# Kernel tuning notes

Measured on AMD Instinct MI355X. Metric: run time of the kernel, lower is better.

## Reference

```python
import jax, jax.numpy as jnp
import numpy as np

LMAX = 6; MMAX = 2
C = 128          # num_channels
H = 8            # num_heads
ALPHA = 32       # attn_alpha_channels
VAL = 16         # attn_value_channels (H*VAL == C)
HID = 64         # attn_hidden_channels
FFN = 128        # ffn_hidden_channels
NL = 4           # num_layers
CUTOFF = 12.0; NRBF = 600
AVG_DEG = 23.395238876342773
AVG_NODES = 77.81317
EPS = 1e-16

def _maps():
    idx, ls = [], []
    for l in range(LMAX + 1):
        mm = min(l, MMAX)
        for m in range(-mm, mm + 1):
            idx.append(l * l + l + m); ls.append(l)
    return np.array(idx), np.array(ls)
_M2F_np, _LOF_np = _maps()
M2F = jnp.asarray(_M2F_np)   # [KM] full-coefficient index of each m-restricted coeff
LOF = jnp.asarray(_LOF_np)   # [KM] degree l of each m-restricted coeff
KM = int(_M2F_np.shape[0])   # 29 for lmax=6, mmax=2
KF = (LMAX + 1) ** 2         # 49

def _rbf(d):
    # GaussianSmearing(0, cutoff, NRBF, width_scalar=2.0)
    off = jnp.linspace(0.0, CUTOFF, NRBF)
    coeff = -0.5 / (2.0 * (off[1] - off[0])) ** 2
    return jnp.exp(coeff * (d[:, None] - off) ** 2)

def _envelope(d):
    # PolynomialEnvelope, exponent p=5
    x = d / CUTOFF
    env = 1.0 - 21.0 * x ** 5 + 35.0 * x ** 6 - 15.0 * x ** 7
    return jnp.where(x < 1.0, env, 0.0)

def _rms(x, g):
    # merge-norm over channel dim with learned per-channel scale
    return x * jax.lax.rsqrt(jnp.mean(x * x, axis=-1, keepdims=True) + 1e-6) * g

def _forward(atomic_numbers, edge_index, edge_distance, emb,
             We0, be0, We1, be1, Weproj, gamma1, gamma2,
             Wr0, Wr1, Wrl, Wmsg, Wap, wa, Wg, Wv, Wo,
             Wf1, Wfg, Wf2, Wh1, Wh2):
    N = atomic_numbers.shape[0]
    src, tgt = edge_index[0], edge_index[1]
    rbf = _rbf(edge_distance)            # [E, NRBF]
    env = _envelope(edge_distance)       # [E]
    # node init: atom embedding on the l=0 component
    x = jnp.zeros((N, KF, C), rbf.dtype).at[:, 0, :].set(emb[atomic_numbers])
    # edge-degree embedding: radial MLP -> per-edge coeffs -> scatter to targets
    h = jax.nn.silu(rbf @ We0 + be0)
    h = jax.nn.silu(h @ We1 + be1)
    deg = (h @ Weproj).reshape(-1, KM, C)              # [E, KM, C]
    x = x.at[tgt[:, None], M2F[None, :], :].add(deg / AVG_DEG)
    for i in range(NL):
        # ---- equivariant graph attention ----
        y = _rms(x, gamma1[i])
        ym = y[:, M2F, :]                               # [N, KM, C] m-restricted
        m = jnp.concatenate([ym[src], ym[tgt]], axis=-1)  # [E, KM, 2C]
        m = jnp.einsum('ekc,ch->ekh', m, Wmsg[i])       # [E, KM, HID]
        # radial function, shared across m within each l (use_rad_l_parametrization)
        rad = jax.nn.silu(jax.nn.silu(rbf @ Wr0[i]) @ Wr1[i])
        radl = rad @ Wrl[i]                             # [E, LMAX+1]
        m = m * radl[:, LOF][..., None]
        # attention logits from invariant (l=0) part
        a = jax.nn.silu(m[:, 0, :] @ Wap[i]).reshape(-1, H, ALPHA)
        logits = jnp.einsum('eha,ha->eh', a, wa[i])     # [E, H]
        segmax = jnp.full((N, H), -jnp.inf, logits.dtype).at[tgt].max(logits)
        ex = env[:, None] * jnp.exp(logits - segmax[tgt])  # envelope-masked softmax
        den = jax.ops.segment_sum(ex, tgt, num_segments=N)
        attn = ex / (den[tgt] + EPS)                    # [E, H]
        # SwiGLU-gated equivariant values
        g = jax.nn.silu(m[:, 0, :] @ Wg[i])             # [E, H*VAL]
        v = jnp.einsum('ekh,hv->ekv', m, Wv[i]) * g[:, None, :]
        v = v.reshape(-1, KM, H, VAL) * attn[:, None, :, None]
        agg = jax.ops.segment_sum(v.reshape(-1, KM, H * VAL), tgt, num_segments=N)
        out = jnp.einsum('nkv,vc->nkc', agg, Wo[i])     # [N, KM, C]
        x = x.at[:, M2F, :].add(out)
        # ---- feed-forward (grid-MLP style SwiGLU) ----
        y = _rms(x, gamma2[i])
        gf = jax.nn.silu(y[:, 0, :] @ Wfg[i])           # [N, FFN]
        hf = jnp.einsum('nkc,cf->nkf', y, Wf1[i]) * gf[:, None, :]
        x = x + jnp.einsum('nkf,fc->nkc', hf, Wf2[i])
    # energy head on invariant part, sum-aggregated over nodes
    s = jax.nn.silu(x[:, 0, :] @ Wh1) @ Wh2             # [N, 1]
    return (jnp.sum(s) / AVG_NODES).reshape(1)

def setup_inputs() -> dict:
    key = jax.random.key(0)
    ks = jax.random.split(key, 24)
    N, E = 6000, 120000
    def rn(k, shape, scale=0.05):
        return jax.random.normal(k, shape, dtype=jnp.float32) * scale
    inp = {}
    inp['atomic_numbers'] = jax.random.randint(ks[0], (N,), 0, 128)
    inp['edge_index'] = jax.random.randint(ks[1], (2, E), 0, N)
    inp['edge_distance'] = jax.random.uniform(ks[2], (E,), minval=0.5, maxval=CUTOFF, dtype=jnp.float32)
    inp['emb'] = rn(ks[3], (128, C), 1.0)
    inp['We0'] = rn(ks[4], (NRBF, 128)); inp['be0'] = jnp.zeros((128,), jnp.float32)
    inp['We1'] = rn(ks[5], (128, 128)); inp['be1'] = jnp.zeros((128,), jnp.float32)
    inp['Weproj'] = rn(ks[6], (128, KM * C))
    inp['gamma1'] = jnp.ones((NL, C), jnp.float32)
    inp['gamma2'] = jnp.ones((NL, C), jnp.float32)
    inp['Wr0'] = rn(ks[7], (NL, NRBF, 128))
    inp['Wr1'] = rn(ks[8], (NL, 128, 128))
    inp['Wrl'] = rn(ks[9], (NL, 128, LMAX + 1), 0.1)
    inp['Wmsg'] = rn(ks[10], (NL, 2 * C, HID))
    inp['Wap'] = rn(ks[11], (NL, HID, H * ALPHA))
    inp['wa'] = rn(ks[12], (NL, H, ALPHA))
    inp['Wg'] = rn(ks[13], (NL, HID, H * VAL))
    inp['Wv'] = rn(ks[14], (NL, HID, H * VAL))
    inp['Wo'] = rn(ks[15], (NL, H * VAL, C))
    inp['Wf1'] = rn(ks[16], (NL, C, FFN))
    inp['Wfg'] = rn(ks[17], (NL, C, FFN))
    inp['Wf2'] = rn(ks[18], (NL, FFN, C))
    inp['Wh1'] = rn(ks[19], (C, C))
    inp['Wh2'] = rn(ks[20], (C, 1))
    return inp

def reference(atomic_numbers, edge_index, edge_distance, emb,
              We0, be0, We1, be1, Weproj, gamma1, gamma2,
              Wr0, Wr1, Wrl, Wmsg, Wap, wa, Wg, Wv, Wo,
              Wf1, Wfg, Wf2, Wh1, Wh2):
    return _forward(atomic_numbers, edge_index, edge_distance, emb,
                    We0, be0, We1, be1, Weproj, gamma1, gamma2,
                    Wr0, Wr1, Wrl, Wmsg, Wap, wa, Wg, Wv, Wo,
                    Wf1, Wfg, Wf2, Wh1, Wh2)
```

## Files before the change

kernel.cpp:

```cpp
#include <hip/hip_runtime.h>

#define KM 29
#define GTAB 4096

typedef __bf16 bf16_t;
typedef __bf16 bf16x8 __attribute__((ext_vector_type(8)));
typedef __bf16 bf16x4 __attribute__((ext_vector_type(4)));
typedef float  f32x4  __attribute__((ext_vector_type(4)));
typedef float  f32x2  __attribute__((ext_vector_type(2)));

__device__ __forceinline__ float silu_f(float x){ return x / (1.0f + __expf(-x)); }

__device__ __forceinline__ float wave_reduce_sum(float v){
  #pragma unroll
  for (int s = 1; s < 64; s <<= 1) v += __shfl_xor(v, s);
  return v;
}

__device__ __forceinline__ constexpr int LOF2(int k){
  return (k<1)?0 : (k<4)?1 : (k<9)?2 : (k<14)?3 : (k<19)?4 : (k<24)?5 : 6;
}

__device__ __forceinline__ f32x4 mfma16(bf16x8 a, bf16x8 b, f32x4 c){
  return __builtin_amdgcn_mfma_f32_16x16x32_bf16(a, b, c, 0, 0, 0);
}

__device__ __forceinline__ float env_f(float d){
  float xx = d*(1.0f/12.0f);
  float x2 = xx*xx, x4 = x2*x2, x5 = x4*xx;
  float env = 1.0f - 21.0f*x5 + 35.0f*x5*xx - 15.0f*x5*x2;
  return (xx < 1.0f) ? env : 0.0f;
}

__global__ void k_count(const int* __restrict__ EI, int* __restrict__ cnt, int E){
  int e = blockIdx.x*256 + threadIdx.x;
  if (e < E) atomicAdd(&cnt[EI[E+e]], 1);
}

__global__ __launch_bounds__(1024) void k_scan(int* __restrict__ cnt, int* __restrict__ rowptr, int N){
  __shared__ int ts[1024];
  int t = threadIdx.x;
  int base = t*8;
  int loc[8]; int sum = 0;
  #pragma unroll
  for (int u = 0; u < 8; u++){ int idx = base+u; int v = (idx < N) ? cnt[idx] : 0; loc[u] = sum; sum += v; }
  ts[t] = sum; __syncthreads();
  for (int off = 1; off < 1024; off <<= 1){
    int v = (t >= off) ? ts[t-off] : 0;
    __syncthreads();
    ts[t] += v;
    __syncthreads();
  }
  int excl = ts[t] - sum;
  #pragma unroll
  for (int u = 0; u < 8; u++){
    int idx = base+u;
    if (idx < N){ int r = excl + loc[u]; rowptr[idx] = r; cnt[idx] = r; }
  }
  if (t == 1023) rowptr[N] = ts[1023];
}

__global__ void k_fill(const int* __restrict__ EI, int* __restrict__ cur, int* __restrict__ order, int E){
  int e = blockIdx.x*256 + threadIdx.x;
  if (e < E){ int pos = atomicAdd(&cur[EI[E+e]], 1); order[pos] = e; }
}

__global__ void k_sort(const int* __restrict__ rowptr, int* __restrict__ order, int N){
  int n = blockIdx.x*256 + threadIdx.x;
  if (n >= N) return;
  int rp = rowptr[n], re = rowptr[n+1];
  for (int a = rp+1; a < re; a++){
    int key = order[a]; int b = a-1;
    while (b >= rp && order[b] > key){ order[b+1] = order[b]; b--; }
    order[b+1] = key;
  }
}

__global__ void k_tr(const float* __restrict__ src, bf16_t* __restrict__ dst,
                     int L, int R, int C, int Lstr){
  int idx = blockIdx.x*256 + threadIdx.x;
  int total = L*R*C;
  if (idx >= total) return;
  int l = idx / (R*C); int rem = idx - l*(R*C);
  int r = rem / C; int c = rem - r*C;
  dst[((size_t)l*C + c)*R + r] = (bf16_t)src[(size_t)l*Lstr + (size_t)r*C + c];
}

__global__ void k_tr2(const float* __restrict__ src, bf16_t* __restrict__ dst){
  int idx = blockIdx.x*256 + threadIdx.x;
  if (idx >= 4*128*128) return;
  int l = idx >> 14; int j = (idx >> 7) & 127; int c = idx & 127;
  float v = (j < 64) ? src[(size_t)l*16384 + c*64 + j]
                     : src[(size_t)l*16384 + 8192 + c*64 + (j-64)];
  dst[idx] = (bf16_t)v;
}

__global__ __launch_bounds__(256) void k_tab_embed(
    const float* __restrict__ We0, const float* __restrict__ be0,
    const float* __restrict__ We1, const float* __restrict__ be1,
    const float* __restrict__ Wr0, const float* __restrict__ Wr1, const float* __restrict__ Wrl,
    float* __restrict__ h2tab, float* __restrict__ radtab)
{
  __shared__ float sb[4][640];
  const int wid = threadIdx.x >> 6, lane = threadIdx.x & 63;
  const int e = blockIdx.x*4 + wid;
  if (e >= GTAB) return;
  const float d = e * (12.0f/(GTAB-1));
  const float DLT = 12.0f/599.0f;
  const float CO  = -0.5f/((2.0f*DLT)*(2.0f*DLT));
  int jc = (int)(d/DLT + 0.5f);
  int j0 = jc - 16; if (j0 < 0) j0 = 0; if (j0 > 600-32) j0 = 600-32;
  float diff = d - (float)(j0+lane)*DLT;
  float gval = __expf(CO*diff*diff);
  float p[10];
  #pragma unroll
  for (int u = 0; u < 10; u++) p[u] = 0.f;
  const int c2 = 2*lane;
  for (int jj = 0; jj < 32; jj++){
    float gj = __shfl(gval, jj);
    int row = j0 + jj;
    const float2 w0 = *(const float2*)(We0 + row*128 + c2);
    p[0] += gj*w0.x; p[1] += gj*w0.y;
    #pragma unroll
    for (int i = 0; i < 4; i++){
      const float2 wr = *(const float2*)(Wr0 + ((size_t)i*600 + row)*128 + c2);
      p[2+2*i] += gj*wr.x; p[3+2*i] += gj*wr.y;
    }
  }
  sb[wid][c2]   = silu_f(p[0] + be0[c2]);
  sb[wid][c2+1] = silu_f(p[1] + be0[c2+1]);
  #pragma unroll
  for (int i = 0; i < 4; i++){
    sb[wid][128 + 128*i + c2]   = silu_f(p[2+2*i]);
    sb[wid][128 + 128*i + c2+1] = silu_f(p[3+2*i]);
  }
  float a0 = 0.f, a1 = 0.f;
  for (int c = 0; c < 128; c++){
    float hv = sb[wid][c];
    const float2 w = *(const float2*)(We1 + c*128 + c2);
    a0 += hv*w.x; a1 += hv*w.y;
  }
  a0 = silu_f(a0 + be1[c2]); a1 = silu_f(a1 + be1[c2+1]);
  h2tab[(size_t)e*128 + c2]     = a0;
  h2tab[(size_t)e*128 + c2 + 1] = a1;
  #pragma unroll
  for (int i = 0; i < 4; i++){
    float r0 = 0.f, r1 = 0.f;
    const float* W1 = Wr1 + (size_t)i*128*128;
    for (int c = 0; c < 128; c++){
      float rv = sb[wid][128 + 128*i + c];
      const float2 w = *(const float2*)(W1 + c*128 + c2);
      r0 += rv*w.x; r1 += rv*w.y;
    }
    r0 = silu_f(r0); r1 = silu_f(r1);
    const float* Wl = Wrl + (size_t)i*128*7;
    float pl[7];
    #pragma unroll
    for (int l = 0; l < 7; l++) pl[l] = r0*Wl[c2*7+l] + r1*Wl[(c2+1)*7+l];
    #pragma unroll
    for (int l = 0; l < 7; l++) pl[l] = wave_reduce_sum(pl[l]);
    if (lane == 0){
      #pragma unroll
      for (int l = 0; l < 7; l++) radtab[(size_t)e*28 + i*7 + l] = pl[l];
    }
  }
}

__global__ void k_h2e(const float* __restrict__ ed, const float* __restrict__ h2tab,
                      bf16_t* __restrict__ h2e, int E){
  int idx = blockIdx.x*256 + threadIdx.x;
  if (idx >= E*128) return;
  int e = idx >> 7, ch = idx & 127;
  float d = ed[e];
  float u = d * ((GTAB-1)/12.0f);
  int j = (int)u; if (j > GTAB-2) j = GTAB-2;
  float f = u - (float)j;
  float a = h2tab[(size_t)j*128 + ch], b = h2tab[(size_t)(j+1)*128 + ch];
  h2e[idx] = (bf16_t)(a + f*(b-a));
}

__global__ __launch_bounds__(256) void k_init_x(
    const int* __restrict__ Z, const float* __restrict__ emb,
    const bf16_t* __restrict__ WeprojT, const bf16_t* __restrict__ h2e,
    const int* __restrict__ rowptr, const int* __restrict__ order,
    float* __restrict__ X, int N)
{
  __shared__ bf16_t h2s[32*136];
  __shared__ int Zs[32];
  int n0 = blockIdx.x*32, t = threadIdx.x;
  int half = t >> 7, ch = t & 127;
  for (int pair = 0; pair < 16; pair++){
    int nn = pair*2 + half;
    int n = n0 + nn;
    float acc = 0.f;
    if (n < N){
      int rp = rowptr[n], deg = rowptr[n+1]-rp;
      for (int idx = 0; idx < deg; idx++){
        int e = order[rp+idx];
        acc += (float)h2e[(size_t)e*128 + ch];
      }
    }
    h2s[nn*136 + ch] = (bf16_t)acc;
  }
  if (t < 32) Zs[t] = (n0 + t < N) ? Z[n0+t] : 0;
  __syncthreads();
  int wid = t >> 6, lane = t & 63;
  int mtile = wid & 1;
  int row = mtile*16 + (lane & 15);
  int koff = (lane >> 4)*8;
  bf16x8 afr[4];
  #pragma unroll
  for (int kk = 0; kk < 4; kk++) afr[kk] = *(const bf16x8*)(h2s + row*136 + kk*32 + koff);
  for (int nt = (wid>>1); nt < 232; nt += 2){
    f32x4 acc = {0.f,0.f,0.f,0.f};
    int col = nt*16 + (lane & 15);
    #pragma unroll
    for (int kk = 0; kk < 4; kk++){
      bf16x8 b = *(const bf16x8*)(WeprojT + (size_t)col*128 + kk*32 + koff);
      acc = mfma16(afr[kk], b, acc);
    }
    #pragma unroll
    for (int r = 0; r < 4; r++){
      int r32 = mtile*16 + (lane>>4)*4 + r;
      int n = n0 + r32;
      if (n < N){
        float v = acc[r] * (1.0f/23.395238876342773f);
        if (col < 128) v += emb[(size_t)Zs[r32]*128 + col];
        X[(size_t)n*3712 + col] = v;
      }
    }
  }
}

__global__ __launch_bounds__(512) void k_pqv(
    const float* __restrict__ X, const float* __restrict__ gamma1,
    const bf16_t* __restrict__ WmsgCT, const bf16_t* __restrict__ WvT,
    unsigned char* __restrict__ PV8, bf16_t* __restrict__ qmb,
    float* __restrict__ P0, float* __restrict__ Q0, int layer)
{
  __shared__ bf16_t ys16[32*136];
  __shared__ bf16_t pq16[32*136];
  int n = blockIdx.x, t = threadIdx.x;
  int wid = t >> 6, lane = t & 63;
  const float* g1 = gamma1 + layer*128;
  const float* xp = X + (size_t)n*3712;
  for (int k = wid; k < KM; k += 8){
    float x0 = xp[k*128 + lane], x1 = xp[k*128 + 64 + lane];
    float ss = wave_reduce_sum(x0*x0 + x1*x1);
    float sc = rsqrtf(ss*(1.0f/128.0f) + 1e-6f);
    ys16[k*136 + lane]      = (bf16_t)(x0*sc*g1[lane]);
    ys16[k*136 + 64 + lane] = (bf16_t)(x1*sc*g1[64+lane]);
  }
  for (int idx = t; idx < 3*136; idx += 512) ys16[29*136 + idx] = (bf16_t)0.f;
  __syncthreads();
  int mtile = wid >> 2;
  int row = mtile*16 + (lane & 15);
  int koff = (lane >> 4)*8;
  {
    const bf16_t* Bc = WmsgCT + (size_t)layer*16384;
    f32x4 acc[2] = {{0,0,0,0},{0,0,0,0}};
    #pragma unroll
    for (int kk = 0; kk < 128; kk += 32){
      bf16x8 a = *(const bf16x8*)(ys16 + row*136 + kk + koff);
      #pragma unroll
      for (int u = 0; u < 2; u++){
        int col = ((wid&3)*2+u)*16 + (lane & 15);
        bf16x8 b = *(const bf16x8*)(Bc + (size_t)col*128 + kk + koff);
        acc[u] = mfma16(a, b, acc[u]);
      }
    }
    #pragma unroll
    for (int u = 0; u < 2; u++){
      int col = ((wid&3)*2+u)*16 + (lane & 15);
      #pragma unroll
      for (int r = 0; r < 4; r++){
        int r32 = mtile*16 + (lane>>4)*4 + r;
        pq16[r32*136 + col] = (bf16_t)acc[u][r];
      }
      if (mtile == 0 && (lane>>4) == 0){
        float v = acc[u][0];
        if (col < 64) P0[(size_t)n*64 + col] = v;
        else          Q0[(size_t)n*64 + col - 64] = v;
      }
    }
  }
  __syncthreads();
  {
    const bf16_t* Bt = WvT + (size_t)layer*8192;
    f32x4 acc[2] = {{0,0,0,0},{0,0,0,0}};
    #pragma unroll
    for (int kk = 0; kk < 64; kk += 32){
      bf16x8 a = *(const bf16x8*)(pq16 + row*136 + kk + koff);
      #pragma unroll
      for (int u = 0; u < 2; u++){
        int col = ((wid&3)*2+u)*16 + (lane & 15);
        bf16x8 b = *(const bf16x8*)(Bt + (size_t)col*64 + kk + koff);
        acc[u] = mfma16(a, b, acc[u]);
      }
    }
    unsigned char* pvp = PV8 + (size_t)n*4096;
    int r0i = mtile*16 + (lane>>4)*4;
    #pragma unroll
    for (int u = 0; u < 2; u++){
      int col = ((wid&3)*2+u)*16 + (lane & 15);
      float pk[4];
      #pragma unroll
      for (int r = 0; r < 4; r++){
        int r32 = r0i + r;
        pk[r] = (r32 < KM) ? acc[u][r] : 0.f;
      }
      int dw = __builtin_amdgcn_cvt_pk_fp8_f32(pk[0], pk[1], 0, false);
      dw = __builtin_amdgcn_cvt_pk_fp8_f32(pk[2], pk[3], dw, true);
      *(unsigned int*)(pvp + col*32 + r0i) = (unsigned int)dw;
    }
  }
  for (int idx = t; idx < KM*64; idx += 512){
    int k = idx >> 6, j = idx & 63;
    qmb[(size_t)n*1856 + idx] = pq16[k*136 + 64 + j];
  }
}

__global__ __launch_bounds__(256) void k_edge_logits(
    const int* __restrict__ EI, const float* __restrict__ ed,
    const float* __restrict__ P0, const float* __restrict__ Q0,
    const float* __restrict__ radtab, const bf16_t* __restrict__ WapT, const float* __restrict__ wa,
    const bf16_t* __restrict__ WgT, float* __restrict__ logi, bf16_t* __restrict__ gate16,
    int E, int layer)
{
  __shared__ bf16_t m0s[16*72];
  __shared__ int   srcs[16], tgts[16];
  __shared__ float r0s[16];
  int t = threadIdx.x;
  int eb = blockIdx.x*16;
  if (t < 16){
    int e = eb + t;
    if (e < E){
      srcs[t] = EI[e]; tgts[t] = EI[E+e];
      float d = ed[e];
      float u = d * ((GTAB-1)/12.0f);
      int j = (int)u; if (j > GTAB-2) j = GTAB-2;
      float f = u - (float)j;
      float a = radtab[(size_t)j*28 + layer*7], b = radtab[(size_t)(j+1)*28 + layer*7];
      r0s[t] = a + f*(b-a);
    } else { srcs[t] = 0; tgts[t] = 0; r0s[t] = 0.f; }
  }
  __syncthreads();
  #pragma unroll
  for (int u = 0; u < 4; u++){
    int idx = t + u*256;
    int i = idx >> 6, j = idx & 63;
    m0s[i*72 + j] = (bf16_t)((P0[(size_t)srcs[i]*64 + j] + Q0[(size_t)tgts[i]*64 + j]) * r0s[i]);
  }
  __syncthreads();
  int wid = t >> 6, lane = t & 63;
  int l15 = lane & 15, lg = lane >> 4;
  int koff = lg*8;
  bf16x8 a0 = *(const bf16x8*)(m0s + l15*72 + koff);
  bf16x8 a1 = *(const bf16x8*)(m0s + l15*72 + 32 + koff);
  const bf16_t* Ba = WapT + (size_t)layer*16384;
  const bf16_t* Bg = WgT  + (size_t)layer*8192;
  const float* wav = wa + layer*256;
  f32x4 accA[4], accG[2];
  #pragma unroll
  for (int u = 0; u < 4; u++){
    int col = 64*wid + u*16 + l15;
    f32x4 acc = {0,0,0,0};
    acc = mfma16(a0, *(const bf16x8*)(Ba + (size_t)col*64 + koff), acc);
    acc = mfma16(a1, *(const bf16x8*)(Ba + (size_t)col*64 + 32 + koff), acc);
    accA[u] = acc;
  }
  #pragma unroll
  for (int u = 0; u < 2; u++){
    int col = 32*wid + u*16 + l15;
    f32x4 acc = {0,0,0,0};
    acc = mfma16(a0, *(const bf16x8*)(Bg + (size_t)col*64 + koff), acc);
    acc = mfma16(a1, *(const bf16x8*)(Bg + (size_t)col*64 + 32 + koff), acc);
    accG[u] = acc;
  }
  #pragma unroll
  for (int u = 0; u < 2; u++){
    int col = 32*wid + u*16 + l15;
    #pragma unroll
    for (int r = 0; r < 4; r++){
      int e = eb + lg*4 + r;
      if (e < E) gate16[(size_t)e*128 + col] = (bf16_t)silu_f(accG[u][r]);
    }
  }
  #pragma unroll
  for (int hpair = 0; hpair < 2; hpair++){
    int c0 = 64*wid + hpair*32 + l15;
    float w0 = wav[c0], w1 = wav[c0+16];
    float s[4];
    #pragma unroll
    for (int r = 0; r < 4; r++)
      s[r] = silu_f(accA[2*hpair][r])*w0 + silu_f(accA[2*hpair+1][r])*w1;
    #pragma unroll
    for (int r = 0; r < 4; r++){
      s[r] += __shfl_xor(s[r], 1);
      s[r] += __shfl_xor(s[r], 2);
      s[r] += __shfl_xor(s[r], 4);
      s[r] += __shfl_xor(s[r], 8);
    }
    if (l15 == 0){
      #pragma unroll
      for (int r = 0; r < 4; r++){
        int e = eb + lg*4 + r;
        if (e < E) logi[(size_t)e*8 + 2*wid + hpair] = s[r];
      }
    }
  }
}

#define FMA_DW(dw, kb) { \
  f32x2 lo_ = __builtin_amdgcn_cvt_pk_f32_fp8((dw), false); \
  f32x2 hi_ = __builtin_amdgcn_cvt_pk_f32_fp8((dw), true); \
  acc[(kb)]   += lo_.x * rw[LOF2((kb))]; \
  acc[(kb)+1] += lo_.y * rw[LOF2((kb)+1)]; \
  acc[(kb)+2] += hi_.x * rw[LOF2((kb)+2)]; \
  acc[(kb)+3] += hi_.y * rw[LOF2((kb)+3)]; }

__global__ __launch_bounds__(512, 4) void k_attn_ffn(
    const int* __restrict__ EI, const int* __restrict__ rowptr, const int* __restrict__ order,
    const float* __restrict__ ed, const bf16_t* __restrict__ qmb,
    const bf16_t* __restrict__ WvT, const bf16_t* __restrict__ WoT,
    const unsigned char* __restrict__ PV8, const bf16_t* __restrict__ gate16,
    const float* __restrict__ logi, const float* __restrict__ radtab,
    const float* __restrict__ gamma2, const float* __restrict__ Wfg,
    const bf16_t* __restrict__ Wf1T, const bf16_t* __restrict__ Wf2T,
    float* __restrict__ X, int layer)
{
  __shared__ float  xs[3712];
  __shared__ bf16_t ysag[32*136];
  __shared__ bf16_t hsqv[32*136];
  __shared__ char   uA[4608];
  __shared__ float  mh[8], iden[8];

  bf16_t* qm16 = (bf16_t*)uA;
  float*  at8  = (float*)uA;
  float*  rl7  = (float*)(uA + 2048);
  int*    es   = (int*)(uA + 4096);
  int*    srcs = (int*)(uA + 4352);
  float*  pf   = (float*)uA;

  int n = blockIdx.x, t = threadIdx.x;
  int wid = t >> 6, lane = t & 63;
  int rp = rowptr[n], deg = rowptr[n+1] - rp;

  for (int idx = t; idx < 3712; idx += 512) xs[idx] = X[(size_t)n*3712 + idx];

  if (deg > 0){
    for (int idx = t; idx < KM*64; idx += 512){
      int k = idx >> 6, j = idx & 63;
      qm16[k*72 + j] = qmb[(size_t)n*1856 + idx];
    }
    for (int idx = t; idx < 3*72; idx += 512) qm16[29*72 + idx] = (bf16_t)0.f;
    if (t < 64){
      int hh = t & 7, slot = t >> 3;
      float m = -3.0e38f;
      for (int idx = slot; idx < deg; idx += 8){
        int e = order[rp+idx];
        m = fmaxf(m, logi[(size_t)e*8 + hh]);
      }
      m = fmaxf(m, __shfl_xor(m, 8));
      m = fmaxf(m, __shfl_xor(m, 16));
      m = fmaxf(m, __shfl_xor(m, 32));
      float den = 0.f;
      for (int idx = slot; idx < deg; idx += 8){
        int e = order[rp+idx];
        den += env_f(ed[e]) * __expf(logi[(size_t)e*8 + hh] - m);
      }
      den += __shfl_xor(den, 8);
      den += __shfl_xor(den, 16);
      den += __shfl_xor(den, 32);
      if (t < 8){ mh[t] = m; iden[t] = 1.0f/(den + 1e-16f); }
    }
    __syncthreads();
    {
      const bf16_t* Bt = WvT + (size_t)layer*8192;
      int mtile = wid >> 2, colt = (wid & 3)*2;
      int row = mtile*16 + (lane & 15);
      int koff = (lane >> 4)*8;
      f32x4 a2[2] = {{0,0,0,0},{0,0,0,0}};
      #pragma unroll
      for (int kk = 0; kk < 64; kk += 32){
        bf16x8 a = *(const bf16x8*)(qm16 + row*72 + kk + koff);
        #pragma unroll
        for (int u = 0; u < 2; u++){
          int col = (colt+u)*16 + (lane & 15);
          bf16x8 b = *(const bf16x8*)(Bt + (size_t)col*64 + kk + koff);
          a2[u] = mfma16(a, b, a2[u]);
        }
      }
      #pragma unroll
      for (int u = 0; u < 2; u++){
        int col = (colt+u)*16 + (lane & 15);
        #pragma unroll
        for (int r = 0; r < 4; r++){
          int r32 = mtile*16 + (lane>>4)*4 + r;
          hsqv[r32*136 + col] = (bf16_t)a2[u][r];
        }
      }
    }
    __syncthreads();
    int eg = t >> 7, hv = t & 127, h = hv >> 4;
    float acc[32];
    #pragma unroll
    for (int j = 0; j < 32; j++) acc[j] = 0.f;
    float S[7];
    #pragma unroll
    for (int l = 0; l < 7; l++) S[l] = 0.f;
    for (int base = 0; base < deg; base += 64){
      int ne = min(64, deg - base);
      if (t < ne){ int e = order[rp + base + t]; es[t] = e; srcs[t] = EI[e]; }
      __syncthreads();
      if (t < ne*8){
        int i = t >> 3, q = t & 7;
        int e = es[i];
        float d = ed[e];
        at8[t] = env_f(d) * __expf(logi[(size_t)e*8 + q] - mh[q]) * iden[q];
        if (q < 7){
          float u = d * ((GTAB-1)/12.0f);
          int j = (int)u; if (j > GTAB-2) j = GTAB-2;
          float f = u - (float)j;
          float a = radtab[(size_t)j*28 + layer*7 + q], b = radtab[(size_t)(j+1)*28 + layer*7 + q];
          rl7[t] = a + f*(b-a);
        }
      }
      __syncthreads();
      uint4 A0 = {0,0,0,0}, A1 = {0,0,0,0}, B0 = {0,0,0,0}, B1 = {0,0,0,0};
      float gA = 0.f, gB = 0.f;
      int i = eg;
      if (i < ne){
        const uint4* p = (const uint4*)(PV8 + (size_t)srcs[i]*4096 + hv*32);
        A0 = p[0]; A1 = p[1];
        gA = (float)gate16[(size_t)es[i]*128 + hv];
      }
      if (i + 4 < ne){
        const uint4* p = (const uint4*)(PV8 + (size_t)srcs[i+4]*4096 + hv*32);
        B0 = p[0]; B1 = p[1];
        gB = (float)gate16[(size_t)es[i+4]*128 + hv];
      }
      while (i < ne){
        int i2 = i + 8;
        uint4 C0 = {0,0,0,0}, C1 = {0,0,0,0}; float gC = 0.f;
        if (i2 < ne){
          const uint4* p = (const uint4*)(PV8 + (size_t)srcs[i2]*4096 + hv*32);
          C0 = p[0]; C1 = p[1];
          gC = (float)gate16[(size_t)es[i2]*128 + hv];
        }
        float w = gA * at8[i*8 + h];
        float rw[7];
        #pragma unroll
        for (int l = 0; l < 7; l++){ rw[l] = rl7[i*8 + l]*w; S[l] += rw[l]; }
        FMA_DW(A0.x, 0)  FMA_DW(A0.y, 4)  FMA_DW(A0.z, 8)  FMA_DW(A0.w, 12)
        FMA_DW(A1.x, 16) FMA_DW(A1.y, 20) FMA_DW(A1.z, 24) FMA_DW(A1.w, 28)
        A0 = B0; A1 = B1; gA = gB;
        B0 = C0; B1 = C1; gB = gC;
        i += 4;
      }
      __syncthreads();
    }
    #pragma unroll
    for (int j = 0; j < 32; j++)
      acc[j] += (float)hsqv[j*136 + hv] * S[LOF2(j)];
    __syncthreads();
    if (eg == 0){
      #pragma unroll
      for (int j = 0; j < 32; j++) ysag[j*136 + hv] = (bf16_t)acc[j];
    } else if (eg == 1){
      #pragma unroll
      for (int j = 0; j < 32; j++) hsqv[j*136 + hv] = (bf16_t)acc[j];
    }
    __syncthreads();
    if (eg == 2){
      #pragma unroll
      for (int j = 0; j < 32; j++) ysag[j*136 + hv] = (bf16_t)((float)ysag[j*136 + hv] + acc[j]);
    } else if (eg == 3){
      #pragma unroll
      for (int j = 0; j < 32; j++) hsqv[j*136 + hv] = (bf16_t)((float)hsqv[j*136 + hv] + acc[j]);
    }
    __syncthreads();
    for (int idx = t; idx < 32*128; idx += 512){
      int k = idx >> 7, c = idx & 127;
      ysag[k*136 + c] = (bf16_t)((float)ysag[k*136 + c] + (float)hsqv[k*136 + c]);
    }
    __syncthreads();
    {
      const bf16_t* Bt = WoT + (size_t)layer*16384;
      int mtile = wid >> 2, colt = (wid & 3)*2;
      int row = mtile*16 + (lane & 15);
      int koff = (lane >> 4)*8;
      f32x4 a2[2] = {{0,0,0,0},{0,0,0,0}};
      #pragma unroll
      for (int kk = 0; kk < 128; kk += 32){
        bf16x8 a = *(const bf16x8*)(ysag + row*136 + kk + koff);
        #pragma unroll
        for (int u = 0; u < 2; u++){
          int col = (colt+u)*16 + (lane & 15);
          bf16x8 b = *(const bf16x8*)(Bt + (size_t)col*128 + kk + koff);
          a2[u] = mfma16(a, b, a2[u]);
        }
      }
      #pragma unroll
      for (int u = 0; u < 2; u++){
        int col = (colt+u)*16 + (lane & 15);
        #pragma unroll
        for (int r = 0; r < 4; r++){
          int r32 = mtile*16 + (lane>>4)*4 + r;
          if (r32 < KM) xs[r32*128 + col] += a2[u][r];
        }
      }
    }
  }
  __syncthreads();
  const float* g2 = gamma2 + layer*128;
  for (int k = wid; k < KM; k += 8){
    float x0 = xs[k*128 + lane], x1 = xs[k*128 + 64 + lane];
    float ss = wave_reduce_sum(x0*x0 + x1*x1);
    float sc = rsqrtf(ss*(1.0f/128.0f) + 1e-6f);
    ysag[k*136 + lane]      = (bf16_t)(x0*sc*g2[lane]);
    ysag[k*136 + 64 + lane] = (bf16_t)(x1*sc*g2[64+lane]);
  }
  for (int idx = t; idx < 3*136; idx += 512) ysag[29*136 + idx] = (bf16_t)0.f;
  __syncthreads();
  {
    int part = t >> 7, f = t & 127;
    const float* Wfgp = Wfg + (size_t)layer*16384;
    float p = 0.f;
    for (int c = part*32; c < part*32 + 32; c++) p += (float)ysag[c] * Wfgp[c*128 + f];
    pf[part*128 + f] = p;
  }
  __syncthreads();
  if (t < 128) pf[512 + t] = silu_f(pf[t] + pf[128+t] + pf[256+t] + pf[384+t]);
  __syncthreads();
  {
    const bf16_t* Bt = Wf1T + (size_t)layer*16384;
    int mtile = wid >> 2, colt = (wid & 3)*2;
    int row = mtile*16 + (lane & 15);
    int koff = (lane >> 4)*8;
    f32x4 a2[2] = {{0,0,0,0},{0,0,0,0}};
    #pragma unroll
    for (int kk = 0; kk < 128; kk += 32){
      bf16x8 a = *(const bf16x8*)(ysag + row*136 + kk + koff);
      #pragma unroll
      for (int u = 0; u < 2; u++){
        int col = (colt+u)*16 + (lane & 15);
        bf16x8 b = *(const bf16x8*)(Bt + (size_t)col*128 + kk + koff);
        a2[u] = mfma16(a, b, a2[u]);
      }
    }
    #pragma unroll
    for (int u = 0; u < 2; u++){
      int col = (colt+u)*16 + (lane & 15);
      float gfc = pf[512 + col];
      #pragma unroll
      for (int r = 0; r < 4; r++){
        int r32 = mtile*16 + (lane>>4)*4 + r;
        hsqv[r32*136 + col] = (bf16_t)(a2[u][r]*gfc);
      }
    }
  }
  __syncthreads();
  {
    const bf16_t* Bt = Wf2T + (size_t)layer*16384;
    int mtile = wid >> 2, colt = (wid & 3)*2;
    int row = mtile*16 + (lane & 15);
    int koff = (lane >> 4)*8;
    f32x4 a2[2] = {{0,0,0,0},{0,0,0,0}};
    #pragma unroll
    for (int kk = 0; kk < 128; kk += 32){
      bf16x8 a = *(const bf16x8*)(hsqv + row*136 + kk + koff);
      #pragma unroll
      for (int u = 0; u < 2; u++){
        int col = (colt+u)*16 + (lane & 15);
        bf16x8 b = *(const bf16x8*)(Bt + (size_t)col*128 + kk + koff);
        a2[u] = mfma16(a, b, a2[u]);
      }
    }
    #pragma unroll
    for (int u = 0; u < 2; u++){
      int col = (colt+u)*16 + (lane & 15);
      #pragma unroll
      for (int r = 0; r < 4; r++){
        int r32 = mtile*16 + (lane>>4)*4 + r;
        if (r32 < KM) xs[r32*128 + col] += a2[u][r];
      }
    }
  }
  __syncthreads();
  for (int idx = t; idx < 3712; idx += 512) X[(size_t)n*3712 + idx] = xs[idx];
}

__global__ __launch_bounds__(256) void k_head(
    const float* __restrict__ X, const float* __restrict__ Wh1, const float* __restrict__ Wh2,
    float* __restrict__ partial, int N)
{
  __shared__ float wsum[4];
  int t = threadIdx.x;
  int half = t >> 7;
  int n = blockIdx.x*2 + half;
  int f = t & 127;
  float sv = 0.f;
  if (n < N){
    const float* xp = X + (size_t)n*3712;
    float acc = 0.f;
    for (int c = 0; c < 128; c++) acc += xp[c]*Wh1[c*128 + f];
    sv = silu_f(acc)*Wh2[f];
  }
  sv = wave_reduce_sum(sv);
  if ((t & 63) == 0) wsum[t >> 6] = sv;
  __syncthreads();
  if (t == 0) partial[blockIdx.x] = wsum[0] + wsum[1] + wsum[2] + wsum[3];
}

__global__ __launch_bounds__(256) void k_reduce(const float* __restrict__ partial, float* __restrict__ out, int P){
  __shared__ float sh[256];
  int t = threadIdx.x;
  float s = 0.f;
  for (int i = t; i < P; i += 256) s += partial[i];
  sh[t] = s; __syncthreads();
  for (int off = 128; off > 0; off >>= 1){
    if (t < off) sh[t] += sh[t+off];
    __syncthreads();
  }
  if (t == 0) out[0] = sh[0] / 77.81317f;
}

extern "C" void kernel_launch(void* const* d_in, const int* in_sizes, int n_in,
                              void* d_out, int out_size, void* d_ws, size_t ws_size,
                              hipStream_t stream)
{
  const int*   Z      = (const int*)d_in[0];
  const int*   EI     = (const int*)d_in[1];
  const float* ed     = (const float*)d_in[2];
  const float* emb    = (const float*)d_in[3];
  const float* We0    = (const float*)d_in[4];
  const float* be0    = (const float*)d_in[5];
  const float* We1    = (const float*)d_in[6];
  const float* be1    = (const float*)d_in[7];
  const float* Weproj = (const float*)d_in[8];
  const float* gamma1 = (const float*)d_in[9];
  const float* gamma2 = (const float*)d_in[10];
  const float* Wr0    = (const float*)d_in[11];
  const float* Wr1    = (const float*)d_in[12];
  const float* Wrl    = (const float*)d_in[13];
  const float* Wmsg   = (const float*)d_in[14];
  const float* Wap    = (const float*)d_in[15];
  const float* wa     = (const float*)d_in[16];
  const float* Wg     = (const float*)d_in[17];
  const float* Wv     = (const float*)d_in[18];
  const float* Wo     = (const float*)d_in[19];
  const float* Wf1    = (const float*)d_in[20];
  const float* Wfg    = (const float*)d_in[21];
  const float* Wf2    = (const float*)d_in[22];
  const float* Wh1    = (const float*)d_in[23];
  const float* Wh2    = (const float*)d_in[24];

  const int N = in_sizes[0];
  const int E = in_sizes[2];

  float* ws = (float*)d_ws;
  size_t o = 0;
  auto alloc = [&](size_t nf){ float* p = ws + o; o += (nf + 7) & ~(size_t)7; return p; };

  float* X      = alloc((size_t)N*3712);
  float* P0     = alloc((size_t)N*64);
  float* Q0     = alloc((size_t)N*64);
  float* logi   = alloc((size_t)E*8);
  float* part   = alloc((size_t)((N+1)/2) + 8);
  float* radtab = alloc((size_t)GTAB*28);
  bf16_t* qmb   = (bf16_t*)alloc((size_t)N*928);
  float* h2tab  = (float*)qmb;
  unsigned char* PV8 = (unsigned char*)alloc((size_t)N*1024);
  bf16_t* gate16= (bf16_t*)alloc((size_t)E*64);
  bf16_t* arena = (bf16_t*)alloc(434176);
  int* rowptr = (int*)alloc((size_t)N+8);
  int* curs   = (int*)alloc((size_t)N);
  int* order  = (int*)alloc((size_t)E);

  bf16_t* WmsgCT  = arena;
  bf16_t* WvT     = arena + 65536;
  bf16_t* WoT     = arena + 98304;
  bf16_t* Wf1T    = arena + 163840;
  bf16_t* Wf2T    = arena + 229376;
  bf16_t* WapT    = arena + 294912;
  bf16_t* WgT     = arena + 360448;
  bf16_t* WeprojT = arena + 393216;

  bf16_t* h2e = gate16;

  hipMemsetAsync(curs, 0, sizeof(int)*N, stream);
  k_count<<<(E+255)/256, 256, 0, stream>>>(EI, curs, E);
  k_scan<<<1, 1024, 0, stream>>>(curs, rowptr, N);
  k_fill<<<(E+255)/256, 256, 0, stream>>>(EI, curs, order, E);
  k_sort<<<(N+255)/256, 256, 0, stream>>>(rowptr, order, N);

  k_tr2<<<256, 256, 0, stream>>>(Wmsg, WmsgCT);
  k_tr<<<128, 256, 0, stream>>>(Wv,   WvT,  4, 64, 128, 8192);
  k_tr<<<256, 256, 0, stream>>>(Wo,   WoT,  4, 128, 128, 16384);
  k_tr<<<256, 256, 0, stream>>>(Wf1,  Wf1T, 4, 128, 128, 16384);
  k_tr<<<256, 256, 0, stream>>>(Wf2,  Wf2T, 4, 128, 128, 16384);
  k_tr<<<256, 256, 0, stream>>>(Wap,  WapT, 4, 64, 256, 16384);
  k_tr<<<128, 256, 0, stream>>>(Wg,   WgT,  4, 64, 128, 8192);
  k_tr<<<1856, 256, 0, stream>>>(Weproj, WeprojT, 1, 128, 3712, 0);

  k_tab_embed<<<GTAB/4, 256, 0, stream>>>(We0, be0, We1, be1, Wr0, Wr1, Wrl, h2tab, radtab);
  k_h2e<<<(E*128+255)/256, 256, 0, stream>>>(ed, h2tab, h2e, E);
  k_init_x<<<(N+31)/32, 256, 0, stream>>>(Z, emb, WeprojT, h2e, rowptr, order, X, N);

  for (int i = 0; i < 4; i++){
    k_pqv<<<N, 512, 0, stream>>>(X, gamma1, WmsgCT, WvT, PV8, qmb, P0, Q0, i);
    k_edge_logits<<<(E+15)/16, 256, 0, stream>>>(EI, ed, P0, Q0, radtab, WapT, wa, WgT, logi, gate16, E, i);
    k_attn_ffn<<<N, 512, 0, stream>>>(EI, rowptr, order, ed, qmb, WvT, WoT, PV8, gate16,
                                      logi, radtab, gamma2, Wfg, Wf1T, Wf2T, X, i);
  }

  int PB = (N+1)/2;
  k_head<<<PB, 256, 0, stream>>>(X, Wh1, Wh2, part, N);
  k_reduce<<<1, 256, 0, stream>>>(part, (float*)d_out, PB);
}
```

Before: 2.409 ms.

## Store node state in bf16 and fuse next-layer projections into attention kernel

```diff
diff --git a/kernel.cpp b/kernel.cpp
--- a/kernel.cpp
+++ b/kernel.cpp
@@ -1,11 +1,12 @@
 #include <hip/hip_runtime.h>
 
 #define KM 29
-#define GTAB 4096
+#define GTAB 2048
 
 typedef __bf16 bf16_t;
 typedef __bf16 bf16x8 __attribute__((ext_vector_type(8)));
 typedef __bf16 bf16x4 __attribute__((ext_vector_type(4)));
+typedef __bf16 bf16x2 __attribute__((ext_vector_type(2)));
 typedef float  f32x4  __attribute__((ext_vector_type(4)));
 typedef float  f32x2  __attribute__((ext_vector_type(2)));
 
@@ -183,7 +184,7 @@
     const int* __restrict__ Z, const float* __restrict__ emb,
     const bf16_t* __restrict__ WeprojT, const bf16_t* __restrict__ h2e,
     const int* __restrict__ rowptr, const int* __restrict__ order,
-    float* __restrict__ X, int N)
+    bf16_t* __restrict__ Xb, int N)
 {
   __shared__ bf16_t h2s[32*136];
   __shared__ int Zs[32];
@@ -226,14 +227,14 @@
       if (n < N){
         float v = acc[r] * (1.0f/23.395238876342773f);
         if (col < 128) v += emb[(size_t)Zs[r32]*128 + col];
-        X[(size_t)n*3712 + col] = v;
+        Xb[(size_t)n*3712 + col] = (bf16_t)v;
       }
     }
   }
 }
 
 __global__ __launch_bounds__(512) void k_pqv(
-    const float* __restrict__ X, const float* __restrict__ gamma1,
+    const bf16_t* __restrict__ Xb, const float* __restrict__ gamma1,
     const bf16_t* __restrict__ WmsgCT, const bf16_t* __restrict__ WvT,
     unsigned char* __restrict__ PV8, bf16_t* __restrict__ qmb,
     float* __restrict__ P0, float* __restrict__ Q0, int layer)
@@ -243,9 +244,9 @@
   int n = blockIdx.x, t = threadIdx.x;
   int wid = t >> 6, lane = t & 63;
   const float* g1 = gamma1 + layer*128;
-  const float* xp = X + (size_t)n*3712;
+  const bf16_t* xp = Xb + (size_t)n*3712;
   for (int k = wid; k < KM; k += 8){
-    float x0 = xp[k*128 + lane], x1 = xp[k*128 + 64 + lane];
+    float x0 = (float)xp[k*128 + lane], x1 = (float)xp[k*128 + 64 + lane];
     float ss = wave_reduce_sum(x0*x0 + x1*x1);
     float sc = rsqrtf(ss*(1.0f/128.0f) + 1e-6f);
     ys16[k*136 + lane]      = (bf16_t)(x0*sc*g1[lane]);
@@ -427,7 +428,10 @@
     const float* __restrict__ logi, const float* __restrict__ radtab,
     const float* __restrict__ gamma2, const float* __restrict__ Wfg,
     const bf16_t* __restrict__ Wf1T, const bf16_t* __restrict__ Wf2T,
-    float* __restrict__ X, int layer)
+    bf16_t* __restrict__ Xb, int layer,
+    const float* __restrict__ gamma1, const bf16_t* __restrict__ WmsgCT,
+    unsigned char* __restrict__ PV8o, bf16_t* __restrict__ qmbo,
+    float* __restrict__ P0o, float* __restrict__ Q0o, int do_tail)
 {
   __shared__ float  xs[3712];
   __shared__ bf16_t ysag[32*136];
@@ -446,7 +450,14 @@
   int wid = t >> 6, lane = t & 63;
   int rp = rowptr[n], deg = rowptr[n+1] - rp;
 
-  for (int idx = t; idx < 3712; idx += 512) xs[idx] = X[(size_t)n*3712 + idx];
+  {
+    const bf16x2* Xp2 = (const bf16x2*)(Xb + (size_t)n*3712);
+    for (int p = t; p < 1856; p += 512){
+      bf16x2 v = Xp2[p];
+      xs[2*p]   = (float)v.x;
+      xs[2*p+1] = (float)v.y;
+    }
+  }
 
   if (deg > 0){
     for (int idx = t; idx < KM*64; idx += 512){
@@ -688,11 +699,95 @@
     }
   }
   __syncthreads();
-  for (int idx = t; idx < 3712; idx += 512) X[(size_t)n*3712 + idx] = xs[idx];
+  {
+    bf16x2* Xp2 = (bf16x2*)(Xb + (size_t)n*3712);
+    for (int p = t; p < 1856; p += 512){
+      bf16x2 v;
+      v.x = (bf16_t)xs[2*p];
+      v.y = (bf16_t)xs[2*p+1];
+      Xp2[p] = v;
+    }
+  }
+  if (do_tail){
+    const float* g1n = gamma1 + (size_t)(layer+1)*128;
+    for (int k = wid; k < KM; k += 8){
+      float x0 = xs[k*128 + lane], x1 = xs[k*128 + 64 + lane];
+      float ss = wave_reduce_sum(x0*x0 + x1*x1);
+      float sc = rsqrtf(ss*(1.0f/128.0f) + 1e-6f);
+      ysag[k*136 + lane]      = (bf16_t)(x0*sc*g1n[lane]);
+      ysag[k*136 + 64 + lane] = (bf16_t)(x1*sc*g1n[64+lane]);
+    }
+    __syncthreads();
+    int mtile = wid >> 2;
+    int row = mtile*16 + (lane & 15);
+    int koff = (lane >> 4)*8;
+    {
+      const bf16_t* Bc = WmsgCT + (size_t)(layer+1)*16384;
+      f32x4 acc[2] = {{0,0,0,0},{0,0,0,0}};
+      #pragma unroll
+      for (int kk = 0; kk < 128; kk += 32){
+        bf16x8 a = *(const bf16x8*)(ysag + row*136 + kk + koff);
+        #pragma unroll
+        for (int u = 0; u < 2; u++){
+          int col = ((wid&3)*2+u)*16 + (lane & 15);
+          bf16x8 b = *(const bf16x8*)(Bc + (size_t)col*128 + kk + koff);
+          acc[u] = mfma16(a, b, acc[u]);
+        }
+      }
+      #pragma unroll
+      for (int u = 0; u < 2; u++){
+        int col = ((wid&3)*2+u)*16 + (lane & 15);
+        #pragma unroll
+        for (int r = 0; r < 4; r++){
+          int r32 = mtile*16 + (lane>>4)*4 + r;
+          hsqv[r32*136 + col] = (bf16_t)acc[u][r];
+        }
+        if (mtile == 0 && (lane>>4) == 0){
+          float v = acc[u][0];
+          if (col < 64) P0o[(size_t)n*64 + col] = v;
+          else          Q0o[(size_t)n*64 + col - 64] = v;
+        }
+      }
+    }
+    __syncthreads();
+    {
+      const bf16_t* Bt = WvT + (size_t)(layer+1)*8192;
+      f32x4 acc[2] = {{0,0,0,0},{0,0,0,0}};
+      #pragma unroll
+      for (int kk = 0; kk < 64; kk += 32){
+        bf16x8 a = *(const bf16x8*)(hsqv + row*136 + kk + koff);
+        #pragma unroll
+        for (int u = 0; u < 2; u++){
+          int col = ((wid&3)*2+u)*16 + (lane & 15);
+          bf16x8 b = *(const bf16x8*)(Bt + (size_t)col*64 + kk + koff);
+          acc[u] = mfma16(a, b, acc[u]);
+        }
+      }
+      unsigned char* pvp = PV8o + (size_t)n*4096;
+      int r0i = mtile*16 + (lane>>4)*4;
+      #pragma unroll
+      for (int u = 0; u < 2; u++){
+        int col = ((wid&3)*2+u)*16 + (lane & 15);
+        float pk[4];
+        #pragma unroll
+        for (int r = 0; r < 4; r++){
+          int r32 = r0i + r;
+          pk[r] = (r32 < KM) ? acc[u][r] : 0.f;
+        }
+        int dw = __builtin_amdgcn_cvt_pk_fp8_f32(pk[0], pk[1], 0, false);
+        dw = __builtin_amdgcn_cvt_pk_fp8_f32(pk[2], pk[3], dw, true);
+        *(unsigned int*)(pvp + col*32 + r0i) = (unsigned int)dw;
+      }
+    }
+    for (int idx = t; idx < KM*64; idx += 512){
+      int k = idx >> 6, j = idx & 63;
+      qmbo[(size_t)n*1856 + idx] = hsqv[k*136 + 64 + j];
+    }
+  }
 }
 
 __global__ __launch_bounds__(256) void k_head(
-    const float* __restrict__ X, const float* __restrict__ Wh1, const float* __restrict__ Wh2,
+    const bf16_t* __restrict__ Xb, const float* __restrict__ Wh1, const float* __restrict__ Wh2,
     float* __restrict__ partial, int N)
 {
   __shared__ float wsum[4];
@@ -702,9 +797,9 @@
   int f = t & 127;
   float sv = 0.f;
   if (n < N){
-    const float* xp = X + (size_t)n*3712;
+    const bf16_t* xp = Xb + (size_t)n*3712;
     float acc = 0.f;
-    for (int c = 0; c < 128; c++) acc += xp[c]*Wh1[c*128 + f];
+    for (int c = 0; c < 128; c++) acc += (float)xp[c]*Wh1[c*128 + f];
     sv = silu_f(acc)*Wh2[f];
   }
   sv = wave_reduce_sum(sv);
@@ -763,15 +858,15 @@
   size_t o = 0;
   auto alloc = [&](size_t nf){ float* p = ws + o; o += (nf + 7) & ~(size_t)7; return p; };
 
-  float* X      = alloc((size_t)N*3712);
-  float* P0     = alloc((size_t)N*64);
-  float* Q0     = alloc((size_t)N*64);
+  bf16_t* Xb    = (bf16_t*)alloc((size_t)N*1856);
+  float* P0     = alloc((size_t)N*128);
+  float* Q0     = alloc((size_t)N*128);
   float* logi   = alloc((size_t)E*8);
   float* part   = alloc((size_t)((N+1)/2) + 8);
   float* radtab = alloc((size_t)GTAB*28);
-  bf16_t* qmb   = (bf16_t*)alloc((size_t)N*928);
+  bf16_t* qmb   = (bf16_t*)alloc((size_t)N*1856);
   float* h2tab  = (float*)qmb;
-  unsigned char* PV8 = (unsigned char*)alloc((size_t)N*1024);
+  unsigned char* PV8 = (unsigned char*)alloc((size_t)N*2048);
   bf16_t* gate16= (bf16_t*)alloc((size_t)E*64);
   bf16_t* arena = (bf16_t*)alloc(434176);
   int* rowptr = (int*)alloc((size_t)N+8);
@@ -806,16 +901,25 @@
 
   k_tab_embed<<<GTAB/4, 256, 0, stream>>>(We0, be0, We1, be1, Wr0, Wr1, Wrl, h2tab, radtab);
   k_h2e<<<(E*128+255)/256, 256, 0, stream>>>(ed, h2tab, h2e, E);
-  k_init_x<<<(N+31)/32, 256, 0, stream>>>(Z, emb, WeprojT, h2e, rowptr, order, X, N);
+  k_init_x<<<(N+31)/32, 256, 0, stream>>>(Z, emb, WeprojT, h2e, rowptr, order, Xb, N);
+
+  k_pqv<<<N, 512, 0, stream>>>(Xb, gamma1, WmsgCT, WvT, PV8, qmb, P0, Q0, 0);
 
   for (int i = 0; i < 4; i++){
-    k_pqv<<<N, 512, 0, stream>>>(X, gamma1, WmsgCT, WvT, PV8, qmb, P0, Q0, i);
-    k_edge_logits<<<(E+15)/16, 256, 0, stream>>>(EI, ed, P0, Q0, radtab, WapT, wa, WgT, logi, gate16, E, i);
-    k_attn_ffn<<<N, 512, 0, stream>>>(EI, rowptr, order, ed, qmb, WvT, WoT, PV8, gate16,
-                                      logi, radtab, gamma2, Wfg, Wf1T, Wf2T, X, i);
+    int cur = i & 1, nxt = (i+1) & 1;
+    unsigned char* PV8i = PV8 + (size_t)cur*N*4096;
+    unsigned char* PV8o = PV8 + (size_t)nxt*N*4096;
+    bf16_t* qmbi = qmb + (size_t)cur*N*1856;
+    bf16_t* qmbo = qmb + (size_t)nxt*N*1856;
+    float* P0i = P0 + (size_t)cur*N*64, *P0o = P0 + (size_t)nxt*N*64;
+    float* Q0i = Q0 + (size_t)cur*N*64, *Q0o = Q0 + (size_t)nxt*N*64;
+    k_edge_logits<<<(E+15)/16, 256, 0, stream>>>(EI, ed, P0i, Q0i, radtab, WapT, wa, WgT, logi, gate16, E, i);
+    k_attn_ffn<<<N, 512, 0, stream>>>(EI, rowptr, order, ed, qmbi, WvT, WoT, PV8i, gate16,
+                                      logi, radtab, gamma2, Wfg, Wf1T, Wf2T, Xb, i,
+                                      gamma1, WmsgCT, PV8o, qmbo, P0o, Q0o, (i < 3) ? 1 : 0);
   }
 
   int PB = (N+1)/2;
-  k_head<<<PB, 256, 0, stream>>>(X, Wh1, Wh2, part, N);
+  k_head<<<PB, 256, 0, stream>>>(Xb, Wh1, Wh2, part, N);
   k_reduce<<<1, 256, 0, stream>>>(part, (float*)d_out, PB);
 }
```

New measurement: 2.340 ms. -2.9%, faster.
